# Kernel tuning notes

Measured on AMD Instinct MI355X. Metric: run time of the kernel, lower is better.

The kernel has to match this reference:

```python
import jax, jax.numpy as jnp
import numpy as np
from jax import lax


def setup_inputs() -> dict:
    key = jax.random.key(0)
    k1, k2, k3, k4 = jax.random.split(key, 4)
    B, K, Hp, Wp = 512, 64, 5, 5
    num_classes = 10
    x = jax.random.uniform(k1, (B, 1, 20, 20), dtype=jnp.float32)
    patterns = jax.random.uniform(k2, (K, 1, Hp, Wp), dtype=jnp.float32)
    w2 = jax.random.normal(k3, (1, K), dtype=jnp.float32) * 0.1
    b2 = jnp.zeros((1,), dtype=jnp.float32)
    wf = jax.random.normal(k4, (num_classes, 400), dtype=jnp.float32) * 0.05
    bf = jnp.zeros((num_classes,), dtype=jnp.float32)
    return {"x": x, "patterns": patterns, "w2": w2, "b2": b2, "wf": wf, "bf": bf}


def _geneo1(patterns, x):
    # patterns: (K,1,Hp,Wp), x: (B,1,H,W). Same-padded sliding L1 similarity.
    K, _, Hp, Wp = patterns.shape
    P = Hp * Wp
    xp = jnp.pad(x, ((0, 0), (0, 0), (Hp // 2, Hp // 2), (Wp // 2, Wp // 2)))
    # (B, P, H_out, W_out); C=1 so feature order is row-major over (Hp,Wp),
    # matching torch's unfold(2,Hp,1).unfold(3,Wp,1).reshape(-1).
    patches = lax.conv_general_dilated_patches(xp, (Hp, Wp), (1, 1), "VALID")
    pat = patterns.reshape(K, P)
    # (B,K,H_out,W_out): mean_|p| |pattern - patch|
    diff = jnp.abs(pat[None, :, :, None, None] - patches[:, None, :, :, :]).mean(axis=2)
    return 1.0 - diff


def _channel_wise_max(t):
    B, K, H, W = t.shape
    flat = t.reshape(B, K, H * W)
    idx = jnp.argmax(flat, axis=2)                      # (B,K)
    mask = jax.nn.one_hot(idx, H * W, dtype=flat.dtype) # (B,K,HW)
    return (flat * mask).reshape(B, K, H, W)


def reference(x, patterns, w2, b2, wf, bf):
    Fk = _geneo1(patterns, x)            # (B,K,20,20)
    cwm = _channel_wise_max(Fk)          # (B,K,20,20)
    # GENEO2: Linear(K,1) over channel dim (applied on (B,H,W,K))
    t = jnp.einsum("bkhw,ok->bhwo", cwm, w2) + b2   # (B,20,20,1)
    t = jax.nn.sigmoid(t)
    out = t.reshape(t.shape[0], -1) @ wf.T + bf      # (B,num_classes)
    return jax.nn.sigmoid(out)
```

## Files before the change

kernel.cpp:

```cpp
#include <hip/hip_runtime.h>
#include <math.h>

#define NB 512
#define NK 64
#define NP 25
#define HW 400
#define NC 10
#define NWAVE 4
#define RPW 5

__global__ __launch_bounds__(256) void geneo_mlp_kernel(
    const float* __restrict__ x,
    const float* __restrict__ patterns,
    const float* __restrict__ w2,
    const float* __restrict__ b2,
    const float* __restrict__ wf,
    const float* __restrict__ bf,
    float* __restrict__ out)
{
    __shared__ __align__(16) float xp[24 * 24];
    __shared__ float  redv[NWAVE][NK];
    __shared__ int    redi[NWAVE][NK];
    __shared__ float2 contrib[NK];
    __shared__ float  wsum[NWAVE][NC];

    const int tid  = threadIdx.x;
    const int b    = blockIdx.x;
    const int lane = tid & 63;
    const int wave = tid >> 6;

    for (int i = tid; i < 24 * 24; i += 256) {
        const int h = i / 24, w = i % 24;
        float v = 0.f;
        if (h >= 2 && h < 22 && w >= 2 && w < 22)
            v = x[b * HW + (h - 2) * 20 + (w - 2)];
        xp[i] = v;
    }

    float patv[NP];
    #pragma unroll
    for (int j = 0; j < NP; ++j) patv[j] = patterns[lane * NP + j];
    __syncthreads();

    float bv = -1e30f;
    int   bi = 0;

    #pragma unroll 1
    for (int r = 0; r < RPW; ++r) {
        const int h = wave * RPW + r;

        float Wn[5][8];
        #pragma unroll
        for (int q = 0; q < 5; ++q) {
            const float4 a = *reinterpret_cast<const float4*>(&xp[(h + q) * 24 + 0]);
            const float4 c = *reinterpret_cast<const float4*>(&xp[(h + q) * 24 + 4]);
            Wn[q][0] = a.x; Wn[q][1] = a.y; Wn[q][2] = a.z; Wn[q][3] = a.w;
            Wn[q][4] = c.x; Wn[q][5] = c.y; Wn[q][6] = c.z; Wn[q][7] = c.w;
        }

        #pragma unroll
        for (int cb = 0; cb < 5; ++cb) {
            #pragma unroll
            for (int px = 0; px < 4; ++px) {
                float s = 0.f;
                #pragma unroll
                for (int dy = 0; dy < 5; ++dy)
                    #pragma unroll
                    for (int dx = 0; dx < 5; ++dx)
                        s += fabsf(patv[dy * 5 + dx] - Wn[dy][px + dx]);
                const float F = 1.f - s * (1.f / 25.f);
                const int   p = h * 20 + cb * 4 + px;
                if (F > bv) { bv = F; bi = p; }
            }
            if (cb < 4) {
                #pragma unroll
                for (int q = 0; q < 5; ++q) {
                    Wn[q][0] = Wn[q][4]; Wn[q][1] = Wn[q][5];
                    Wn[q][2] = Wn[q][6]; Wn[q][3] = Wn[q][7];
                    const float4 nb = *reinterpret_cast<const float4*>(
                        &xp[(h + q) * 24 + cb * 4 + 8]);
                    Wn[q][4] = nb.x; Wn[q][5] = nb.y; Wn[q][6] = nb.z; Wn[q][7] = nb.w;
                }
            }
        }
    }
    redv[wave][lane] = bv;
    redi[wave][lane] = bi;
    __syncthreads();

    if (tid < NK) {
        float v0 = redv[0][tid];
        int   i0 = redi[0][tid];
        #pragma unroll
        for (int w = 1; w < NWAVE; ++w) {
            const float ov = redv[w][tid];
            const int   oi = redi[w][tid];
            if (ov > v0) { v0 = ov; i0 = oi; }
        }
        contrib[tid] = make_float2(v0 * w2[tid], __int_as_float(i0));
    }
    __syncthreads();

    float acc[NC];
    #pragma unroll
    for (int c = 0; c < NC; ++c) acc[c] = 0.f;
    const float b2v = b2[0];

    {
        const int p0 = tid;
        float s = b2v;
        for (int k = 0; k < NK; ++k) {
            const float2 cv = contrib[k];
            if (__float_as_int(cv.y) == p0) s += cv.x;
        }
        const float t = 1.f / (1.f + expf(-s));
        #pragma unroll
        for (int c = 0; c < NC; ++c) acc[c] += t * wf[c * HW + p0];
    }
    if (tid + 256 < HW) {
        const int p1 = tid + 256;
        float s = b2v;
        for (int k = 0; k < NK; ++k) {
            const float2 cv = contrib[k];
            if (__float_as_int(cv.y) == p1) s += cv.x;
        }
        const float t = 1.f / (1.f + expf(-s));
        #pragma unroll
        for (int c = 0; c < NC; ++c) acc[c] += t * wf[c * HW + p1];
    }

    #pragma unroll
    for (int c = 0; c < NC; ++c) {
        #pragma unroll
        for (int off = 32; off >= 1; off >>= 1)
            acc[c] += __shfl_down(acc[c], off);
    }
    if (lane == 0) {
        #pragma unroll
        for (int c = 0; c < NC; ++c) wsum[wave][c] = acc[c];
    }
    __syncthreads();
    if (tid < NC) {
        const float s = wsum[0][tid] + wsum[1][tid] + wsum[2][tid] + wsum[3][tid] + bf[tid];
        out[b * NC + tid] = 1.f / (1.f + expf(-s));
    }
}

extern "C" void kernel_launch(void* const* d_in, const int* in_sizes, int n_in,
                              void* d_out, int out_size, void* d_ws, size_t ws_size,
                              hipStream_t stream) {
    const float* x        = (const float*)d_in[0];
    const float* patterns = (const float*)d_in[1];
    const float* w2       = (const float*)d_in[2];
    const float* b2       = (const float*)d_in[3];
    const float* wf       = (const float*)d_in[4];
    const float* bf       = (const float*)d_in[5];
    float* out = (float*)d_out;

    geneo_mlp_kernel<<<NB, 256, 0, stream>>>(x, patterns, w2, b2, wf, bf, out);
}
```

Measured before the change: 20.52 us.

## Split each row across two waves with 512-thread blocks and min-sum tracking

Doubles the block to 8 waves so each pair of waves handles one group of rows, with each wave covering half of a 20-pixel row. Each wave now loads a 16-wide register window once per row instead of sliding it in float4 steps. The running argmax becomes an argmin on the raw L1 sum, so the 1 - s/25 conversion happens once after the cross-wave reduction, and ties go to the lower index. The aim is more parallel waves per image and less per-thread work; the cost is higher register pressure from the bigger window, plus the launch_bounds occupancy hint.

```diff
diff --git a/kernel.cpp b/kernel.cpp
--- a/kernel.cpp
+++ b/kernel.cpp
@@ -6,10 +6,26 @@
 #define NP 25
 #define HW 400
 #define NC 10
-#define NWAVE 4
-#define RPW 5
+#define NWAVE 8
 
-__global__ __launch_bounds__(256) void geneo_mlp_kernel(
+template<int WOFF>
+__device__ __forceinline__ void row10(const float (&Wf)[5][16], const float (&patv)[NP],
+                                      int sbase, float& smin, int& bi)
+{
+    #pragma unroll
+    for (int px = 0; px < 10; ++px) {
+        float s = 0.f;
+        #pragma unroll
+        for (int dy = 0; dy < 5; ++dy)
+            #pragma unroll
+            for (int dx = 0; dx < 5; ++dx)
+                s += fabsf(patv[dy * 5 + dx] - Wf[dy][WOFF + px + dx]);
+        const int p = sbase + px;
+        if (s < smin) { smin = s; bi = p; }
+    }
+}
+
+__global__ __launch_bounds__(512, 4) void geneo_mlp_kernel(
     const float* __restrict__ x,
     const float* __restrict__ patterns,
     const float* __restrict__ w2,
@@ -28,8 +44,10 @@
     const int b    = blockIdx.x;
     const int lane = tid & 63;
     const int wave = tid >> 6;
+    const int rw   = wave >> 1;
+    const int ch   = wave & 1;
 
-    for (int i = tid; i < 24 * 24; i += 256) {
+    for (int i = tid; i < 24 * 24; i += 512) {
         const int h = i / 24, w = i % 24;
         float v = 0.f;
         if (h >= 2 && h < 22 && w >= 2 && w < 22)
@@ -42,49 +60,31 @@
     for (int j = 0; j < NP; ++j) patv[j] = patterns[lane * NP + j];
     __syncthreads();
 
-    float bv = -1e30f;
-    int   bi = 0;
+    float smin = 1e30f;
+    int   bi   = 0;
 
     #pragma unroll 1
-    for (int r = 0; r < RPW; ++r) {
-        const int h = wave * RPW + r;
+    for (int r = 0; r < 5; ++r) {
+        const int h = rw * 5 + r;
 
-        float Wn[5][8];
+        float Wf[5][16];
         #pragma unroll
         for (int q = 0; q < 5; ++q) {
-            const float4 a = *reinterpret_cast<const float4*>(&xp[(h + q) * 24 + 0]);
-            const float4 c = *reinterpret_cast<const float4*>(&xp[(h + q) * 24 + 4]);
-            Wn[q][0] = a.x; Wn[q][1] = a.y; Wn[q][2] = a.z; Wn[q][3] = a.w;
-            Wn[q][4] = c.x; Wn[q][5] = c.y; Wn[q][6] = c.z; Wn[q][7] = c.w;
+            const float* rp = &xp[(h + q) * 24 + ch * 8];
+            const float4 a = *reinterpret_cast<const float4*>(rp + 0);
+            const float4 c = *reinterpret_cast<const float4*>(rp + 4);
+            const float4 d = *reinterpret_cast<const float4*>(rp + 8);
+            const float4 e = *reinterpret_cast<const float4*>(rp + 12);
+            Wf[q][0]  = a.x; Wf[q][1]  = a.y; Wf[q][2]  = a.z; Wf[q][3]  = a.w;
+            Wf[q][4]  = c.x; Wf[q][5]  = c.y; Wf[q][6]  = c.z; Wf[q][7]  = c.w;
+            Wf[q][8]  = d.x; Wf[q][9]  = d.y; Wf[q][10] = d.z; Wf[q][11] = d.w;
+            Wf[q][12] = e.x; Wf[q][13] = e.y; Wf[q][14] = e.z; Wf[q][15] = e.w;
         }
-
-        #pragma unroll
-        for (int cb = 0; cb < 5; ++cb) {
-            #pragma unroll
-            for (int px = 0; px < 4; ++px) {
-                float s = 0.f;
-                #pragma unroll
-                for (int dy = 0; dy < 5; ++dy)
-                    #pragma unroll
-                    for (int dx = 0; dx < 5; ++dx)
-                        s += fabsf(patv[dy * 5 + dx] - Wn[dy][px + dx]);
-                const float F = 1.f - s * (1.f / 25.f);
-                const int   p = h * 20 + cb * 4 + px;
-                if (F > bv) { bv = F; bi = p; }
-            }
-            if (cb < 4) {
-                #pragma unroll
-                for (int q = 0; q < 5; ++q) {
-                    Wn[q][0] = Wn[q][4]; Wn[q][1] = Wn[q][5];
-                    Wn[q][2] = Wn[q][6]; Wn[q][3] = Wn[q][7];
-                    const float4 nb = *reinterpret_cast<const float4*>(
-                        &xp[(h + q) * 24 + cb * 4 + 8]);
-                    Wn[q][4] = nb.x; Wn[q][5] = nb.y; Wn[q][6] = nb.z; Wn[q][7] = nb.w;
-                }
-            }
-        }
+        const int sbase = h * 20 + ch * 10;
+        if (ch == 0) row10<0>(Wf, patv, sbase, smin, bi);
+        else         row10<2>(Wf, patv, sbase, smin, bi);
     }
-    redv[wave][lane] = bv;
+    redv[wave][lane] = smin;
     redi[wave][lane] = bi;
     __syncthreads();
 
@@ -95,38 +95,26 @@
         for (int w = 1; w < NWAVE; ++w) {
             const float ov = redv[w][tid];
             const int   oi = redi[w][tid];
-            if (ov > v0) { v0 = ov; i0 = oi; }
+            if (ov < v0 || (ov == v0 && oi < i0)) { v0 = ov; i0 = oi; }
         }
-        contrib[tid] = make_float2(v0 * w2[tid], __int_as_float(i0));
+        const float F = 1.f - v0 * (1.f / 25.f);
+        contrib[tid] = make_float2(F * w2[tid], __int_as_float(i0));
     }
     __syncthreads();
 
     float acc[NC];
     #pragma unroll
     for (int c = 0; c < NC; ++c) acc[c] = 0.f;
-    const float b2v = b2[0];
 
-    {
-        const int p0 = tid;
-        float s = b2v;
+    if (tid < HW) {
+        float s = b2[0];
         for (int k = 0; k < NK; ++k) {
             const float2 cv = contrib[k];
-            if (__float_as_int(cv.y) == p0) s += cv.x;
+            if (__float_as_int(cv.y) == tid) s += cv.x;
         }
         const float t = 1.f / (1.f + expf(-s));
         #pragma unroll
-        for (int c = 0; c < NC; ++c) acc[c] += t * wf[c * HW + p0];
-    }
-    if (tid + 256 < HW) {
-        const int p1 = tid + 256;
-        float s = b2v;
-        for (int k = 0; k < NK; ++k) {
-            const float2 cv = contrib[k];
-            if (__float_as_int(cv.y) == p1) s += cv.x;
-        }
-        const float t = 1.f / (1.f + expf(-s));
-        #pragma unroll
-        for (int c = 0; c < NC; ++c) acc[c] += t * wf[c * HW + p1];
+        for (int c = 0; c < NC; ++c) acc[c] += t * wf[c * HW + tid];
     }
 
     #pragma unroll
@@ -141,7 +129,9 @@
     }
     __syncthreads();
     if (tid < NC) {
-        const float s = wsum[0][tid] + wsum[1][tid] + wsum[2][tid] + wsum[3][tid] + bf[tid];
+        float s = bf[tid];
+        #pragma unroll
+        for (int w = 0; w < NWAVE; ++w) s += wsum[w][tid];
         out[b * NC + tid] = 1.f / (1.f + expf(-s));
     }
 }
@@ -157,5 +147,5 @@
     const float* bf       = (const float*)d_in[5];
     float* out = (float*)d_out;
 
-    geneo_mlp_kernel<<<NB, 256, 0, stream>>>(x, patterns, w2, b2, wf, bf, out);
+    geneo_mlp_kernel<<<NB, 512, 0, stream>>>(x, patterns, w2, b2, wf, bf, out);
 }
```

New measurement: 60.35 us. 2.94x slower.

## Quantize to 16-bit and compute L1 distances with packed v_sad_u16

Applied to the files above, without the earlier changes.

Inputs and patterns are quantized to 16-bit fixed point and two rows are packed per 32-bit word. The L1 patch distance is then computed with v_sad_u16, which handles two rows per instruction. The argmax is packed as (score<<9 | pixel index) so one unsigned min replaces the float compare-and-select, and patterns are staged through LDS. This trades exact float distances for quantized ones, so near ties in the argmax may resolve differently.

```diff
diff --git a/kernel.cpp b/kernel.cpp
--- a/kernel.cpp
+++ b/kernel.cpp
@@ -6,10 +6,18 @@
 #define NP 25
 #define HW 400
 #define NC 10
-#define NWAVE 4
-#define RPW 5
 
-__global__ __launch_bounds__(256) void geneo_mlp_kernel(
+__device__ __forceinline__ unsigned sad16(unsigned a, unsigned b, unsigned c) {
+#if __has_builtin(__builtin_amdgcn_sad_u16)
+    return __builtin_amdgcn_sad_u16(a, b, c);
+#else
+    unsigned d;
+    asm("v_sad_u16 %0, %1, %2, %3" : "=v"(d) : "v"(a), "v"(b), "v"(c));
+    return d;
+#endif
+}
+
+__global__ void geneo_mlp_kernel(
     const float* __restrict__ x,
     const float* __restrict__ patterns,
     const float* __restrict__ w2,
@@ -18,86 +26,91 @@
     const float* __restrict__ bf,
     float* __restrict__ out)
 {
-    __shared__ __align__(16) float xp[24 * 24];
-    __shared__ float  redv[NWAVE][NK];
-    __shared__ int    redi[NWAVE][NK];
+    __shared__ unsigned xq[24 * 24];
+    __shared__ unsigned pqd[23 * 24];
+    __shared__ __align__(16) float pat_lds[NK * NP];
+    __shared__ unsigned redbest[4][NK];
     __shared__ float2 contrib[NK];
-    __shared__ float  wsum[NWAVE][NC];
+    __shared__ float  wsum[4][NC];
 
     const int tid  = threadIdx.x;
     const int b    = blockIdx.x;
     const int lane = tid & 63;
     const int wave = tid >> 6;
 
-    for (int i = tid; i < 24 * 24; i += 256) {
-        const int h = i / 24, w = i % 24;
+    for (int i = tid; i < 576; i += 256) {
+        const int h = i / 24, w = i - h * 24;
         float v = 0.f;
         if (h >= 2 && h < 22 && w >= 2 && w < 22)
             v = x[b * HW + (h - 2) * 20 + (w - 2)];
-        xp[i] = v;
+        xq[i] = (unsigned)(v * 65535.f + 0.5f);
     }
-
-    float patv[NP];
-    #pragma unroll
-    for (int j = 0; j < NP; ++j) patv[j] = patterns[lane * NP + j];
+    {
+        const float4* p4 = reinterpret_cast<const float4*>(patterns);
+        float4*       l4 = reinterpret_cast<float4*>(pat_lds);
+        l4[tid] = p4[tid];
+        if (tid + 256 < 400) l4[tid + 256] = p4[tid + 256];
+    }
     __syncthreads();
 
-    float bv = -1e30f;
-    int   bi = 0;
+    for (int i = tid; i < 552; i += 256)
+        pqd[i] = xq[i] | (xq[i + 24] << 16);
+
+    unsigned vp01[5], vp23[5], p4v[5];
+    #pragma unroll
+    for (int c = 0; c < 5; ++c) {
+        const unsigned q0 = (unsigned)(pat_lds[lane * NP +  0 + c] * 65535.f + 0.5f);
+        const unsigned q1 = (unsigned)(pat_lds[lane * NP +  5 + c] * 65535.f + 0.5f);
+        const unsigned q2 = (unsigned)(pat_lds[lane * NP + 10 + c] * 65535.f + 0.5f);
+        const unsigned q3 = (unsigned)(pat_lds[lane * NP + 15 + c] * 65535.f + 0.5f);
+        const unsigned q4 = (unsigned)(pat_lds[lane * NP + 20 + c] * 65535.f + 0.5f);
+        vp01[c] = q0 | (q1 << 16);
+        vp23[c] = q2 | (q3 << 16);
+        p4v[c]  = q4;
+    }
+    __syncthreads();
+
+    unsigned best = 0xFFFFFFFFu;
+    const int h0 = wave * 5;
 
     #pragma unroll 1
-    for (int r = 0; r < RPW; ++r) {
-        const int h = wave * RPW + r;
-
-        float Wn[5][8];
-        #pragma unroll
-        for (int q = 0; q < 5; ++q) {
-            const float4 a = *reinterpret_cast<const float4*>(&xp[(h + q) * 24 + 0]);
-            const float4 c = *reinterpret_cast<const float4*>(&xp[(h + q) * 24 + 4]);
-            Wn[q][0] = a.x; Wn[q][1] = a.y; Wn[q][2] = a.z; Wn[q][3] = a.w;
-            Wn[q][4] = c.x; Wn[q][5] = c.y; Wn[q][6] = c.z; Wn[q][7] = c.w;
-        }
-
-        #pragma unroll
-        for (int cb = 0; cb < 5; ++cb) {
+    for (int r = 0; r < 5; ++r) {
+        const int h = h0 + r;
+        #pragma unroll 1
+        for (int cb = 0; cb < 4; ++cb) {
+            const int c0 = cb * 5;
+            const unsigned* r01 = &pqd[h * 24 + c0];
+            const unsigned* r23 = &pqd[(h + 2) * 24 + c0];
+            const unsigned* r4  = &xq[(h + 4) * 24 + c0];
+            unsigned W01[9], W23[9], W4[9];
             #pragma unroll
-            for (int px = 0; px < 4; ++px) {
-                float s = 0.f;
+            for (int d = 0; d < 9; ++d) {
+                W01[d] = r01[d]; W23[d] = r23[d]; W4[d] = r4[d];
+            }
+            #pragma unroll
+            for (int px = 0; px < 5; ++px) {
+                unsigned s = 0;
                 #pragma unroll
-                for (int dy = 0; dy < 5; ++dy)
-                    #pragma unroll
-                    for (int dx = 0; dx < 5; ++dx)
-                        s += fabsf(patv[dy * 5 + dx] - Wn[dy][px + dx]);
-                const float F = 1.f - s * (1.f / 25.f);
-                const int   p = h * 20 + cb * 4 + px;
-                if (F > bv) { bv = F; bi = p; }
-            }
-            if (cb < 4) {
-                #pragma unroll
-                for (int q = 0; q < 5; ++q) {
-                    Wn[q][0] = Wn[q][4]; Wn[q][1] = Wn[q][5];
-                    Wn[q][2] = Wn[q][6]; Wn[q][3] = Wn[q][7];
-                    const float4 nb = *reinterpret_cast<const float4*>(
-                        &xp[(h + q) * 24 + cb * 4 + 8]);
-                    Wn[q][4] = nb.x; Wn[q][5] = nb.y; Wn[q][6] = nb.z; Wn[q][7] = nb.w;
+                for (int dx = 0; dx < 5; ++dx) {
+                    s = sad16(W01[px + dx], vp01[dx], s);
+                    s = sad16(W23[px + dx], vp23[dx], s);
+                    s = sad16(W4 [px + dx], p4v [dx], s);
                 }
+                const unsigned pk = (s << 9) | (unsigned)(h * 20 + c0 + px);
+                best = min(best, pk);
             }
         }
     }
-    redv[wave][lane] = bv;
-    redi[wave][lane] = bi;
+    redbest[wave][lane] = best;
     __syncthreads();
 
     if (tid < NK) {
-        float v0 = redv[0][tid];
-        int   i0 = redi[0][tid];
-        #pragma unroll
-        for (int w = 1; w < NWAVE; ++w) {
-            const float ov = redv[w][tid];
-            const int   oi = redi[w][tid];
-            if (ov > v0) { v0 = ov; i0 = oi; }
-        }
-        contrib[tid] = make_float2(v0 * w2[tid], __int_as_float(i0));
+        const unsigned b0 = min(min(redbest[0][tid], redbest[1][tid]),
+                                min(redbest[2][tid], redbest[3][tid]));
+        const unsigned s  = b0 >> 9;
+        const int    pix  = (int)(b0 & 511u);
+        const float  F    = 1.f - (float)s * (1.f / (25.f * 65535.f));
+        contrib[tid] = make_float2(F * w2[tid], __int_as_float(pix));
     }
     __syncthreads();
 
```

New measurement: 23.09 us. 1.13x slower.
